# Optimization experiments

Measured on AMD Instinct MI355X. Metric: run time of the kernel, lower is better.

## Reference

```python
import jax, jax.numpy as jnp
import numpy as np

N_QUBITS = 10
BATCH = 16384
Q_DEPTH = 2


def _apply_1q_shared(state, U, q):
    # state: [B, 2, 2, ..., 2]; U: [2, 2] complex, acting on wire q
    state = jnp.moveaxis(state, 1 + q, -1)
    state = jnp.einsum('b...i,ji->b...j', state, U)
    return jnp.moveaxis(state, -1, 1 + q)


def _apply_ry_batched(state, angles, q):
    # per-sample RY(angle) on wire q; angles: [B] float
    c = jnp.cos(angles * 0.5).astype(jnp.complex64)
    s = jnp.sin(angles * 0.5).astype(jnp.complex64)
    U = jnp.stack([jnp.stack([c, -s], -1), jnp.stack([s, c], -1)], -2)  # [B,2,2]
    state = jnp.moveaxis(state, 1 + q, -1)
    state = jnp.einsum('b...i,bji->b...j', state, U)
    return jnp.moveaxis(state, -1, 1 + q)


def _rot_matrix(phi, theta, omega):
    # PennyLane Rot = RZ(omega) @ RY(theta) @ RZ(phi)
    c = jnp.cos(theta * 0.5)
    s = jnp.sin(theta * 0.5)
    m00 = jnp.exp(-0.5j * (phi + omega)) * c
    m01 = -jnp.exp(0.5j * (phi - omega)) * s
    m10 = jnp.exp(-0.5j * (phi - omega)) * s
    m11 = jnp.exp(0.5j * (phi + omega)) * c
    return jnp.stack([jnp.stack([m00, m01]), jnp.stack([m10, m11])]).astype(jnp.complex64)


def _apply_cnot(state, c, t):
    st = jnp.moveaxis(state, (1 + c, 1 + t), (1, 2))  # [B, ctrl, tgt, ...]
    st = jnp.stack([st[:, 0], st[:, 1, ::-1]], axis=1)  # flip target where ctrl=1
    return jnp.moveaxis(st, (1, 2), (1 + c, 1 + t))


def setup_inputs() -> dict:
    key = jax.random.key(0)
    k1, k2 = jax.random.split(key)
    x = jax.random.uniform(k1, (BATCH, N_QUBITS), dtype=jnp.float32) * np.pi
    q_weights = 0.01 * jax.random.normal(k2, (Q_DEPTH, N_QUBITS, 3), dtype=jnp.float32)
    return {"x": x, "q_weights": q_weights}


def reference(x, q_weights) -> jnp.ndarray:
    B, n = x.shape
    L = q_weights.shape[0]
    # |0...0> statevector, batched: [B] + [2]*n (axis q <-> wire q, wire 0 most significant)
    state = jnp.zeros((B, 2 ** n), jnp.complex64).at[:, 0].set(1.0)
    state = state.reshape((B,) + (2,) * n)
    # AngleEmbedding(rotation='Y')
    for q in range(n):
        state = _apply_ry_batched(state, x[:, q], q)
    # StronglyEntanglingLayers: Rot on each wire, then ring of CNOTs with range (l % (n-1)) + 1
    for l in range(L):
        for q in range(n):
            U = _rot_matrix(q_weights[l, q, 0], q_weights[l, q, 1], q_weights[l, q, 2])
            state = _apply_1q_shared(state, U, q)
        r = (l % (n - 1)) + 1
        for q in range(n):
            state = _apply_cnot(state, q, (q + r) % n)
    probs = jnp.abs(state.reshape(B, 2 ** n)) ** 2  # [B, 2^n]
    bits = (np.arange(2 ** n)[:, None] >> (n - 1 - np.arange(n))[None, :]) & 1
    signs = jnp.asarray(1.0 - 2.0 * bits, jnp.float32)  # [2^n, n], PauliZ eigenvalues
    return (probs @ signs).astype(jnp.float32)  # [B, n] expvals
```

## Files before the change

kernel.cpp:

```cpp
#include <hip/hip_runtime.h>

#define DEVINL __device__ __forceinline__

typedef float f32x2 __attribute__((ext_vector_type(2)));

struct GC { int laneXor, regXor, rowL, rowR; };
struct Circ { GC g[20]; int sgnL[10], sgnR[10]; int lsel[5]; };

constexpr Circ build_circ() {
    Circ c{};
    unsigned A[10] = {};
    for (int i = 0; i < 10; ++i) A[i] = 1u << i;
    for (int w = 0; w < 10; ++w) {
        int pos = 9 - w;
        unsigned m = 1u << pos;
        c.g[w] = GC{ int(m >> 5), int(m & 31u), int(m >> 5), int(m & 31u) };
    }
    for (int q = 0; q < 10; ++q) { int pc = 9 - q, pt = 9 - ((q + 1) % 10); A[pt] ^= A[pc]; }
    unsigned M[10] = {}, Inv[10] = {};
    for (int i = 0; i < 10; ++i) { M[i] = A[i]; Inv[i] = 1u << i; }
    for (int col = 0; col < 10; ++col) {
        int piv = col;
        while (!((M[piv] >> col) & 1u)) ++piv;
        unsigned tm = M[col]; M[col] = M[piv]; M[piv] = tm;
        unsigned ti = Inv[col]; Inv[col] = Inv[piv]; Inv[piv] = ti;
        for (int r = 0; r < 10; ++r)
            if (r != col && ((M[r] >> col) & 1u)) { M[r] ^= M[col]; Inv[r] ^= Inv[col]; }
    }
    for (int w = 0; w < 10; ++w) {
        int pos = 9 - w;
        unsigned m = 0;
        for (int i = 0; i < 10; ++i) m |= ((Inv[i] >> pos) & 1u) << i;
        unsigned row = A[pos];
        c.g[10 + w] = GC{ int(m >> 5), int(m & 31u), int(row >> 5), int(row & 31u) };
    }
    for (int q = 0; q < 10; ++q) { int pc = 9 - q, pt = 9 - ((q + 2) % 10); A[pt] ^= A[pc]; }
    for (int q = 0; q < 10; ++q) { unsigned row = A[9 - q]; c.sgnL[q] = int(row >> 5); c.sgnR[q] = int(row & 31u); }

    unsigned Ucols[5] = {};
    {
        unsigned tgt[5] = {16, 8, 7, 2, 1};
        unsigned acc = 0;
        for (int k = 0; k < 5; ++k) { acc ^= tgt[k]; Ucols[k] = acc; }
    }
    unsigned Urows[5] = {};
    for (int r = 0; r < 5; ++r)
        for (int cc = 0; cc < 5; ++cc)
            Urows[r] |= ((Ucols[cc] >> r) & 1u) << cc;
    unsigned MM[5] = {}, AI[5] = {};
    for (int i = 0; i < 5; ++i) { MM[i] = Urows[i]; AI[i] = 1u << i; }
    for (int col = 0; col < 5; ++col) {
        int piv = col;
        while (!((MM[piv] >> col) & 1u)) ++piv;
        unsigned tm = MM[col]; MM[col] = MM[piv]; MM[piv] = tm;
        unsigned ti = AI[col]; AI[col] = AI[piv]; AI[piv] = ti;
        for (int r = 0; r < 5; ++r)
            if (r != col && ((MM[r] >> col) & 1u)) { MM[r] ^= MM[col]; AI[r] ^= AI[col]; }
    }
    for (int w = 0; w < 10; ++w) {
        unsigned mL = unsigned(c.g[10 + w].laneXor);
        unsigned nm = 0;
        for (int i = 0; i < 5; ++i) if ((mL >> i) & 1u) nm ^= Ucols[i];
        c.g[10 + w].laneXor = int(nm);
        unsigned rL = unsigned(c.g[10 + w].rowL);
        unsigned nr = 0;
        for (int i = 0; i < 5; ++i) if ((rL >> i) & 1u) nr ^= AI[i];
        c.g[10 + w].rowL = int(nr);
    }
    for (int q = 0; q < 10; ++q) {
        unsigned sL = unsigned(c.sgnL[q]);
        unsigned ns = 0;
        for (int i = 0; i < 5; ++i) if ((sL >> i) & 1u) ns ^= AI[i];
        c.sgnL[q] = int(ns);
    }
    for (int o = 0; o < 5; ++o) c.lsel[o] = int(AI[o]);
    return c;
}

constexpr Circ CC = build_circ();

static_assert(CC.g[10].laneXor == 1  && CC.g[10].regXor == 0,  "w0");
static_assert(CC.g[11].laneXor == 2  && CC.g[11].regXor == 0,  "w1");
static_assert(CC.g[12].laneXor == 7  && CC.g[12].regXor == 0,  "w2");
static_assert(CC.g[13].laneXor == 8  && CC.g[13].regXor == 0,  "w3");
static_assert(CC.g[14].laneXor == 16 && CC.g[14].regXor == 16, "w4");
static_assert(CC.g[15].laneXor == 0  && CC.g[15].regXor == 24, "w5");
static_assert(CC.g[16].laneXor == 0  && CC.g[16].regXor == 12, "w6");
static_assert(CC.g[17].laneXor == 0  && CC.g[17].regXor == 6,  "w7");
static_assert(CC.g[18].laneXor == 0  && CC.g[18].regXor == 3,  "w8");
static_assert(CC.g[19].laneXor == 1  && CC.g[19].regXor == 1,  "w9");
static_assert(CC.g[10].rowR == 31, "w0 rowR");
static_assert(CC.g[11].rowR == 0,  "w1 rowR");
static_assert(CC.g[12].rowR == 0,  "w2 rowR");
static_assert(CC.g[13].rowR == 0,  "w3 rowR");
static_assert(CC.g[14].rowR == 0,  "w4 rowR");
static_assert(CC.g[15].rowR == 16, "w5 rowR");
static_assert(CC.g[16].rowR == 24, "w6 rowR");
static_assert(CC.g[17].rowR == 28, "w7 rowR");
static_assert(CC.g[18].rowR == 30, "w8 rowR");
static_assert(CC.g[19].rowR == 31, "w9 rowR");

DEVINL float csw(float v, int sw) {
    return __int_as_float(__float_as_int(v) ^ sw);
}

template<int XOR>
DEVINL float fetch(float v, int lane) {
    if constexpr (XOR == 0)      return v;
    else if constexpr (XOR == 1) return __int_as_float(__builtin_amdgcn_update_dpp(0, __float_as_int(v), 0xB1, 0xF, 0xF, true));
    else if constexpr (XOR == 2) return __int_as_float(__builtin_amdgcn_update_dpp(0, __float_as_int(v), 0x4E, 0xF, 0xF, true));
    else if constexpr (XOR == 3) return __int_as_float(__builtin_amdgcn_update_dpp(0, __float_as_int(v), 0x1B, 0xF, 0xF, true));
    else if constexpr (XOR == 7) return __int_as_float(__builtin_amdgcn_update_dpp(0, __float_as_int(v), 0x141, 0xF, 0xF, true));
    else if constexpr (XOR == 8) return __int_as_float(__builtin_amdgcn_update_dpp(0, __float_as_int(v), 0x128, 0xF, 0xF, true));
    else                         return __int_as_float(__builtin_amdgcn_ds_swizzle(__float_as_int(v), 0x1F | (XOR << 10)));
}

DEVINL void pk_fma_acc(f32x2& a, f32x2 t, f32x2 b) {
    asm("v_pk_fma_f32 %0, %1, %2, %0" : "+v"(a) : "v"(t), "v"(b));
}

DEVINL f32x2 cmul(f32x2 a, f32x2 b) {
    f32x2 r;
    r.x = a.x * b.x - a.y * b.y;
    r.y = a.x * b.y + a.y * b.x;
    return r;
}

__device__ __attribute__((aligned(16))) float g_cst[80];

__global__ void qprep(const float* __restrict__ qw) {
    int g = threadIdx.x;
    if (g < 10) {
        float phi = qw[g * 3 + 0], th = qw[g * 3 + 1], om = qw[g * 3 + 2];
        float c = cosf(0.5f * th), s = sinf(0.5f * th);
        float apo = 0.5f * (phi + om), amo = 0.5f * (phi - om);
        g_cst[g * 4 + 0] =  cosf(apo) * c;
        g_cst[g * 4 + 1] = -sinf(apo) * c;
        g_cst[g * 4 + 2] = -cosf(amo) * s;
        g_cst[g * 4 + 3] = -sinf(amo) * s;
    } else if (g < 20) {
        int w = g - 10;
        float phi = qw[g * 3 + 0], th = qw[g * 3 + 1];
        float c = cosf(0.5f * th), s = sinf(0.5f * th);
        g_cst[40 + w] = s / c;
        g_cst[50 + w * 2 + 0] =  cosf(0.5f * phi);
        g_cst[50 + w * 2 + 1] = -sinf(0.5f * phi);
    } else if (g == 20) {
        float p = 1.f;
        for (int w = 0; w < 10; ++w) p *= cosf(0.5f * qw[(10 + w) * 3 + 1]);
        g_cst[70] = p;
    }
}

DEVINL void wf(const float* cst, float xw, int w, f32x2& f0, f32x2& f1) {
    float h = 0.5f * xw;
    float s = __sinf(h), c = __cosf(h);
    float m0 = cst[w * 4 + 0], m1 = cst[w * 4 + 1], m2 = cst[w * 4 + 2], m3 = cst[w * 4 + 3];
    f0.x =  m0 * c + m2 * s;
    f0.y =  m1 * c + m3 * s;
    f1.x = -m2 * c + m0 * s;
    f1.y =  m3 * c - m1 * s;
}

template<int W>
DEVINL void apply_gate(f32x2 (&a2)[32], const float* cst, int lane, const int (&sw)[10]) {
    constexpr GC gc = CC.g[10 + W];
    float tt = csw(cst[40 + W], sw[W]);
    f32x2 tp; tp.x = tt;  tp.y = tt;
    f32x2 tn; tn.x = -tt; tn.y = -tt;
    if constexpr (gc.laneXor == 0) {
        #pragma unroll
        for (int r = 0; r < 32; ++r) {
            const int r2 = r ^ gc.regXor;
            if (r < r2) {
                f32x2 old = a2[r];
                const bool sR  = __builtin_popcount(unsigned(gc.rowR & r )) & 1;
                const bool sR2 = __builtin_popcount(unsigned(gc.rowR & r2)) & 1;
                pk_fma_acc(a2[r],  sR  ? tp : tn, a2[r2]);
                pk_fma_acc(a2[r2], sR2 ? tp : tn, old);
            }
        }
    } else {
        #pragma unroll
        for (int c = 0; c < 2; ++c) {
            f32x2 b2[16];
            #pragma unroll
            for (int i = 0; i < 16; ++i) {
                const int r = (i & 7) + c * 8 + ((i >> 3) << 4);
                f32x2 s = a2[r ^ gc.regXor];
                b2[i].x = fetch<gc.laneXor>(s.x, lane);
                b2[i].y = fetch<gc.laneXor>(s.y, lane);
            }
            #pragma unroll
            for (int i = 0; i < 16; ++i) {
                const int r = (i & 7) + c * 8 + ((i >> 3) << 4);
                const bool sR = __builtin_popcount(unsigned(gc.rowR & r)) & 1;
                pk_fma_acc(a2[r], sR ? tp : tn, b2[i]);
            }
        }
    }
}

__global__ __launch_bounds__(256) void qsim(const float* __restrict__ x,
                                            float* __restrict__ out, int B) {
    const float* cst = g_cst;
    int lane = threadIdx.x & 63;
    int l5 = lane & 31;
    int b = blockIdx.x * 8 + (threadIdx.x >> 5);
    if (b >= B) return;
    const float* xb = x + b * 10;

    int sw_[10];
    #pragma unroll
    for (int w = 0; w < 10; ++w)
        sw_[w] = (__popc(unsigned(l5 & CC.g[10 + w].rowL)) & 1) << 31;

    f32x2 t01[4], t23[4], f5t[2];
    {
        f32x2 a0, a1, b0, b1;
        wf(cst, xb[9], 9, a0, a1);
        wf(cst, xb[8], 8, b0, b1);
        t01[0] = cmul(a0, b0); t01[1] = cmul(a1, b0);
        t01[2] = cmul(a0, b1); t01[3] = cmul(a1, b1);
        wf(cst, xb[7], 7, a0, a1);
        wf(cst, xb[6], 6, b0, b1);
        t23[0] = cmul(a0, b0); t23[1] = cmul(a1, b0);
        t23[2] = cmul(a0, b1); t23[3] = cmul(a1, b1);
        wf(cst, xb[5], 5, f5t[0], f5t[1]);
    }

    f32x2 E0; E0.x = cst[50];      E0.y = csw(cst[51], sw_[0]);
    f32x2 E1; E1.x = cst[52];      E1.y = csw(cst[53], sw_[1]);
    f32x2 E2; E2.x = cst[54];      E2.y = csw(cst[55], sw_[2]);
    f32x2 E3; E3.x = cst[56];      E3.y = csw(cst[57], sw_[3]);
    f32x2 E4; E4.x = cst[58];      E4.y = csw(cst[59], sw_[4]);
    f32x2 E5; E5.x = cst[60];      E5.y = csw(cst[61], sw_[5]);
    f32x2 E6; E6.x = cst[62];      E6.y = csw(cst[63], sw_[6]);
    f32x2 E7; E7.x = cst[64];      E7.y = csw(cst[65], sw_[7]);
    f32x2 E8; E8.x = cst[66];      E8.y = csw(cst[67], sw_[8]);
    f32x2 E9; E9.x = cst[68];      E9.y = csw(cst[69], sw_[9]);

    f32x2 lf;
    {
        f32x2 ea = cmul(cmul(E1, E2), cmul(E3, E4));
        float sc = cst[70];
        lf.x = ea.x * sc; lf.y = ea.y * sc;
        #pragma unroll
        for (int jj = 0; jj < 5; ++jj) {
            int w = 4 - jj;
            f32x2 f0, f1;
            wf(cst, xb[w], w, f0, f1);
            int bit = __popc(unsigned(l5 & CC.lsel[jj])) & 1;
            f32x2 p; p.x = bit ? f1.x : f0.x; p.y = bit ? f1.y : f0.y;
            lf = cmul(lf, p);
        }
    }

    f32x2 f5p[2];
    f5p[0] = cmul(f5t[0], E5);
    { f32x2 e5c; e5c.x = E5.x; e5c.y = -E5.y; f5p[1] = cmul(f5t[1], e5c); }
    f32x2 V00 = cmul(E6, E7);
    f32x2 V01; { f32x2 e7c; e7c.x = E7.x; e7c.y = -E7.y; V01 = cmul(E6, e7c); }
    f32x2 EB = cmul(E9, E0);
    f32x2 H0 = cmul(E8, EB);
    f32x2 H1; { f32x2 ebc; ebc.x = EB.x; ebc.y = -EB.y; H1 = cmul(E8, ebc); }

    f32x2 tf[8];
    #pragma unroll
    for (int j = 0; j < 8; ++j) {
        f32x2 tA = cmul(t23[j & 3], f5p[j >> 2]);
        const int s6 = ((j >> 2) ^ (j >> 1)) & 1;
        const int s7 = s6 ^ (j & 1);
        f32x2 V;
        V.x = s6 ? (s7 ? V00.x : V01.x) : (s7 ? V01.x : V00.x);
        V.y = s6 ? -(s7 ? V00.y : V01.y) : (s7 ? V01.y : V00.y);
        tf[j] = cmul(tA, V);
    }

    f32x2 g4[4];
    #pragma unroll
    for (int v = 0; v < 4; ++v) g4[v] = cmul(lf, t01[v]);
    f32x2 a2[32];
    #pragma unroll
    for (int r = 0; r < 32; ++r) {
        f32x2 t = cmul(g4[r & 3], tf[(r >> 2) & 7]);
        f32x2 G;
        G.x = (r & 1) ? H1.x : H0.x;
        G.y = (r & 1) ? H1.y : H0.y;
        if (__builtin_popcount(unsigned(r & 30)) & 1) G.y = -G.y;
        a2[r] = cmul(t, G);
    }

    apply_gate<4>(a2, cst, lane, sw_);
    apply_gate<5>(a2, cst, lane, sw_);
    apply_gate<0>(a2, cst, lane, sw_);
    apply_gate<6>(a2, cst, lane, sw_);
    apply_gate<1>(a2, cst, lane, sw_);
    apply_gate<7>(a2, cst, lane, sw_);
    apply_gate<2>(a2, cst, lane, sw_);
    apply_gate<8>(a2, cst, lane, sw_);
    apply_gate<3>(a2, cst, lane, sw_);
    apply_gate<9>(a2, cst, lane, sw_);

    float wv[32];
    #pragma unroll
    for (int r = 0; r < 32; ++r) wv[r] = a2[r].x * a2[r].x + a2[r].y * a2[r].y;
    #pragma unroll
    for (int bS = 1; bS < 16; bS <<= 1) {
        #pragma unroll
        for (int r = 0; r < 32; ++r) {
            if (!(r & bS)) {
                float xv = wv[r], yv = wv[r | bS];
                wv[r]      = xv + yv;
                wv[r | bS] = xv - yv;
            }
        }
    }

    float e[10];
    #pragma unroll
    for (int q = 0; q < 10; ++q) {
        const int R = CC.sgnR[q];
        float num = (R & 16) ? (wv[R ^ 16] - wv[R]) : (wv[R] + wv[R ^ 16]);
        int slq = __popc(unsigned(l5 & CC.sgnL[q])) & 1;
        e[q] = csw(num, slq << 31);
    }

    #pragma unroll
    for (int q = 0; q < 10; ++q) {
        e[q] += fetch<1>(e[q], lane);
        e[q] += fetch<2>(e[q], lane);
    }
    int s = l5 & 3;
    bool s1 = (s & 1) != 0, s2 = (s & 2) != 0;
    float v0 = s1 ? e[1] : e[0];
    float u0 = s1 ? e[3] : e[2];
    v0 = s2 ? u0 : v0;
    float v1 = s1 ? e[5] : e[4];
    float u1 = s1 ? e[7] : e[6];
    v1 = s2 ? u1 : v1;
    float v2 = s1 ? e[9] : e[8];

    v0 += fetch<4>(v0, lane);   v1 += fetch<4>(v1, lane);   v2 += fetch<4>(v2, lane);
    v0 += fetch<8>(v0, lane);   v1 += fetch<8>(v1, lane);   v2 += fetch<8>(v2, lane);
    v0 += fetch<16>(v0, lane);  v1 += fetch<16>(v1, lane);  v2 += fetch<16>(v2, lane);

    float vo = v0;
    int hi = l5 >> 2;
    vo = (hi == 1) ? v1 : vo;
    vo = (hi == 2) ? v2 : vo;
    if (l5 < 10) out[b * 10 + l5] = vo;
}

extern "C" void kernel_launch(void* const* d_in, const int* in_sizes, int n_in,
                              void* d_out, int out_size, void* d_ws, size_t ws_size,
                              hipStream_t stream) {
    const float* x  = (const float*)d_in[0];
    const float* qw = (const float*)d_in[1];
    float* out = (float*)d_out;
    int B = in_sizes[0] / 10;
    int blocks = (B + 7) / 8;
    hipLaunchKernelGGL(qprep, dim3(1), dim3(64), 0, stream, qw);
    hipLaunchKernelGGL(qsim, dim3(blocks), dim3(256), 0, stream, x, out, B);
}
```

Measured before the change: 84.56 us.

## Spread statevector across full 64-lane wavefront and process two samples per wave

The 1024-amplitude statevector was split as 32 lanes × 32 registers. It is now split as 64 lanes × 16 registers, and each wavefront simulates two batch samples interleaved. The constexpr qubit-to-lane/register mapping is rebuilt for 6 lane bits, and gates that cross the 32-lane boundary use bpermute or permlane32 swaps. The intent is fewer registers per sample and independent work from the second sample to hide cross-lane shuffle latency. The cost is more cross-lane traffic, including slower 32-lane exchanges, and a reduction that runs over 64 lanes.

```diff
diff --git a/kernel.cpp b/kernel.cpp
--- a/kernel.cpp
+++ b/kernel.cpp
@@ -5,7 +5,7 @@
 typedef float f32x2 __attribute__((ext_vector_type(2)));
 
 struct GC { int laneXor, regXor, rowL, rowR; };
-struct Circ { GC g[20]; int sgnL[10], sgnR[10]; int lsel[5]; };
+struct Circ { GC g[20]; int sgnL[10], sgnR[10]; int lsel[6]; };
 
 constexpr Circ build_circ() {
     Circ c{};
@@ -14,7 +14,7 @@
     for (int w = 0; w < 10; ++w) {
         int pos = 9 - w;
         unsigned m = 1u << pos;
-        c.g[w] = GC{ int(m >> 5), int(m & 31u), int(m >> 5), int(m & 31u) };
+        c.g[w] = GC{ int(m >> 4), int(m & 15u), int(m >> 4), int(m & 15u) };
     }
     for (int q = 0; q < 10; ++q) { int pc = 9 - q, pt = 9 - ((q + 1) % 10); A[pt] ^= A[pc]; }
     unsigned M[10] = {}, Inv[10] = {};
@@ -32,48 +32,48 @@
         unsigned m = 0;
         for (int i = 0; i < 10; ++i) m |= ((Inv[i] >> pos) & 1u) << i;
         unsigned row = A[pos];
-        c.g[10 + w] = GC{ int(m >> 5), int(m & 31u), int(row >> 5), int(row & 31u) };
+        c.g[10 + w] = GC{ int(m >> 4), int(m & 15u), int(row >> 4), int(row & 15u) };
     }
     for (int q = 0; q < 10; ++q) { int pc = 9 - q, pt = 9 - ((q + 2) % 10); A[pt] ^= A[pc]; }
-    for (int q = 0; q < 10; ++q) { unsigned row = A[9 - q]; c.sgnL[q] = int(row >> 5); c.sgnR[q] = int(row & 31u); }
-
-    unsigned Ucols[5] = {};
+    for (int q = 0; q < 10; ++q) { unsigned row = A[9 - q]; c.sgnL[q] = int(row >> 4); c.sgnR[q] = int(row & 15u); }
+
+    unsigned Ucols[6] = {};
     {
-        unsigned tgt[5] = {16, 8, 7, 2, 1};
+        unsigned tgt[6] = {32, 16, 7, 8, 2, 1};
         unsigned acc = 0;
-        for (int k = 0; k < 5; ++k) { acc ^= tgt[k]; Ucols[k] = acc; }
-    }
-    unsigned Urows[5] = {};
-    for (int r = 0; r < 5; ++r)
-        for (int cc = 0; cc < 5; ++cc)
+        for (int k = 0; k < 6; ++k) { acc ^= tgt[k]; Ucols[k] = acc; }
+    }
+    unsigned Urows[6] = {};
+    for (int r = 0; r < 6; ++r)
+        for (int cc = 0; cc < 6; ++cc)
             Urows[r] |= ((Ucols[cc] >> r) & 1u) << cc;
-    unsigned MM[5] = {}, AI[5] = {};
-    for (int i = 0; i < 5; ++i) { MM[i] = Urows[i]; AI[i] = 1u << i; }
-    for (int col = 0; col < 5; ++col) {
+    unsigned MM[6] = {}, AI[6] = {};
+    for (int i = 0; i < 6; ++i) { MM[i] = Urows[i]; AI[i] = 1u << i; }
+    for (int col = 0; col < 6; ++col) {
         int piv = col;
         while (!((MM[piv] >> col) & 1u)) ++piv;
         unsigned tm = MM[col]; MM[col] = MM[piv]; MM[piv] = tm;
         unsigned ti = AI[col]; AI[col] = AI[piv]; AI[piv] = ti;
-        for (int r = 0; r < 5; ++r)
+        for (int r = 0; r < 6; ++r)
             if (r != col && ((MM[r] >> col) & 1u)) { MM[r] ^= MM[col]; AI[r] ^= AI[col]; }
     }
     for (int w = 0; w < 10; ++w) {
         unsigned mL = unsigned(c.g[10 + w].laneXor);
         unsigned nm = 0;
-        for (int i = 0; i < 5; ++i) if ((mL >> i) & 1u) nm ^= Ucols[i];
+        for (int i = 0; i < 6; ++i) if ((mL >> i) & 1u) nm ^= Ucols[i];
         c.g[10 + w].laneXor = int(nm);
         unsigned rL = unsigned(c.g[10 + w].rowL);
         unsigned nr = 0;
-        for (int i = 0; i < 5; ++i) if ((rL >> i) & 1u) nr ^= AI[i];
+        for (int i = 0; i < 6; ++i) if ((rL >> i) & 1u) nr ^= AI[i];
         c.g[10 + w].rowL = int(nr);
     }
     for (int q = 0; q < 10; ++q) {
         unsigned sL = unsigned(c.sgnL[q]);
         unsigned ns = 0;
-        for (int i = 0; i < 5; ++i) if ((sL >> i) & 1u) ns ^= AI[i];
+        for (int i = 0; i < 6; ++i) if ((sL >> i) & 1u) ns ^= AI[i];
         c.sgnL[q] = int(ns);
     }
-    for (int o = 0; o < 5; ++o) c.lsel[o] = int(AI[o]);
+    for (int o = 0; o < 6; ++o) c.lsel[o] = int(AI[o]);
     return c;
 }
 
@@ -81,27 +81,41 @@
 
 static_assert(CC.g[10].laneXor == 1  && CC.g[10].regXor == 0,  "w0");
 static_assert(CC.g[11].laneXor == 2  && CC.g[11].regXor == 0,  "w1");
-static_assert(CC.g[12].laneXor == 7  && CC.g[12].regXor == 0,  "w2");
-static_assert(CC.g[13].laneXor == 8  && CC.g[13].regXor == 0,  "w3");
-static_assert(CC.g[14].laneXor == 16 && CC.g[14].regXor == 16, "w4");
-static_assert(CC.g[15].laneXor == 0  && CC.g[15].regXor == 24, "w5");
+static_assert(CC.g[12].laneXor == 8  && CC.g[12].regXor == 0,  "w2");
+static_assert(CC.g[13].laneXor == 7  && CC.g[13].regXor == 0,  "w3");
+static_assert(CC.g[14].laneXor == 16 && CC.g[14].regXor == 0,  "w4");
+static_assert(CC.g[15].laneXor == 32 && CC.g[15].regXor == 8,  "w5");
 static_assert(CC.g[16].laneXor == 0  && CC.g[16].regXor == 12, "w6");
 static_assert(CC.g[17].laneXor == 0  && CC.g[17].regXor == 6,  "w7");
 static_assert(CC.g[18].laneXor == 0  && CC.g[18].regXor == 3,  "w8");
 static_assert(CC.g[19].laneXor == 1  && CC.g[19].regXor == 1,  "w9");
-static_assert(CC.g[10].rowR == 31, "w0 rowR");
+static_assert(CC.g[10].rowR == 15, "w0 rowR");
 static_assert(CC.g[11].rowR == 0,  "w1 rowR");
 static_assert(CC.g[12].rowR == 0,  "w2 rowR");
 static_assert(CC.g[13].rowR == 0,  "w3 rowR");
 static_assert(CC.g[14].rowR == 0,  "w4 rowR");
-static_assert(CC.g[15].rowR == 16, "w5 rowR");
-static_assert(CC.g[16].rowR == 24, "w6 rowR");
-static_assert(CC.g[17].rowR == 28, "w7 rowR");
-static_assert(CC.g[18].rowR == 30, "w8 rowR");
-static_assert(CC.g[19].rowR == 31, "w9 rowR");
+static_assert(CC.g[15].rowR == 0,  "w5 rowR");
+static_assert(CC.g[16].rowR == 8,  "w6 rowR");
+static_assert(CC.g[17].rowR == 12, "w7 rowR");
+static_assert(CC.g[18].rowR == 14, "w8 rowR");
+static_assert(CC.g[19].rowR == 15, "w9 rowR");
+
+#if __has_builtin(__builtin_amdgcn_permlane32_swap)
+#define HAS_PL32 1
+#else
+#define HAS_PL32 0
+#endif
+#if __has_builtin(__builtin_amdgcn_permlane16_swap)
+#define HAS_PL16 1
+#else
+#define HAS_PL16 0
+#endif
 
 DEVINL float csw(float v, int sw) {
     return __int_as_float(__float_as_int(v) ^ sw);
+}
+DEVINL int sgnw(int lane, int rowL) {
+    return (__popc(unsigned(lane & rowL)) & 1) << 31;
 }
 
 template<int XOR>
@@ -112,7 +126,25 @@
     else if constexpr (XOR == 3) return __int_as_float(__builtin_amdgcn_update_dpp(0, __float_as_int(v), 0x1B, 0xF, 0xF, true));
     else if constexpr (XOR == 7) return __int_as_float(__builtin_amdgcn_update_dpp(0, __float_as_int(v), 0x141, 0xF, 0xF, true));
     else if constexpr (XOR == 8) return __int_as_float(__builtin_amdgcn_update_dpp(0, __float_as_int(v), 0x128, 0xF, 0xF, true));
-    else                         return __int_as_float(__builtin_amdgcn_ds_swizzle(__float_as_int(v), 0x1F | (XOR << 10)));
+    else if constexpr (XOR < 32) return __int_as_float(__builtin_amdgcn_ds_swizzle(__float_as_int(v), 0x1F | (XOR << 10)));
+    else                         return __int_as_float(__builtin_amdgcn_ds_bpermute((lane ^ XOR) << 2, __float_as_int(v)));
+}
+
+DEVINL float bsum16(float v, int lane) {
+#if HAS_PL16
+    auto r = __builtin_amdgcn_permlane16_swap(__float_as_int(v), __float_as_int(v), false, false);
+    return __int_as_float(r[0]) + __int_as_float(r[1]);
+#else
+    return v + fetch<16>(v, lane);
+#endif
+}
+DEVINL float bsum32(float v, int lane) {
+#if HAS_PL32
+    auto r = __builtin_amdgcn_permlane32_swap(__float_as_int(v), __float_as_int(v), false, false);
+    return __int_as_float(r[0]) + __int_as_float(r[1]);
+#else
+    return v + fetch<32>(v, lane);
+#endif
 }
 
 DEVINL void pk_fma_acc(f32x2& a, f32x2 t, f32x2 b) {
@@ -152,6 +184,13 @@
     }
 }
 
+DEVINL f32x2 mkE(const float* cst, int w, int lane) {
+    f32x2 E;
+    E.x = cst[50 + w * 2];
+    E.y = csw(cst[50 + w * 2 + 1], sgnw(lane, CC.g[10 + w].rowL));
+    return E;
+}
+
 DEVINL void wf(const float* cst, float xw, int w, f32x2& f0, f32x2& f1) {
     float h = 0.5f * xw;
     float s = __sinf(h), c = __cosf(h);
@@ -162,60 +201,8 @@
     f1.y =  m3 * c - m1 * s;
 }
 
-template<int W>
-DEVINL void apply_gate(f32x2 (&a2)[32], const float* cst, int lane, const int (&sw)[10]) {
-    constexpr GC gc = CC.g[10 + W];
-    float tt = csw(cst[40 + W], sw[W]);
-    f32x2 tp; tp.x = tt;  tp.y = tt;
-    f32x2 tn; tn.x = -tt; tn.y = -tt;
-    if constexpr (gc.laneXor == 0) {
-        #pragma unroll
-        for (int r = 0; r < 32; ++r) {
-            const int r2 = r ^ gc.regXor;
-            if (r < r2) {
-                f32x2 old = a2[r];
-                const bool sR  = __builtin_popcount(unsigned(gc.rowR & r )) & 1;
-                const bool sR2 = __builtin_popcount(unsigned(gc.rowR & r2)) & 1;
-                pk_fma_acc(a2[r],  sR  ? tp : tn, a2[r2]);
-                pk_fma_acc(a2[r2], sR2 ? tp : tn, old);
-            }
-        }
-    } else {
-        #pragma unroll
-        for (int c = 0; c < 2; ++c) {
-            f32x2 b2[16];
-            #pragma unroll
-            for (int i = 0; i < 16; ++i) {
-                const int r = (i & 7) + c * 8 + ((i >> 3) << 4);
-                f32x2 s = a2[r ^ gc.regXor];
-                b2[i].x = fetch<gc.laneXor>(s.x, lane);
-                b2[i].y = fetch<gc.laneXor>(s.y, lane);
-            }
-            #pragma unroll
-            for (int i = 0; i < 16; ++i) {
-                const int r = (i & 7) + c * 8 + ((i >> 3) << 4);
-                const bool sR = __builtin_popcount(unsigned(gc.rowR & r)) & 1;
-                pk_fma_acc(a2[r], sR ? tp : tn, b2[i]);
-            }
-        }
-    }
-}
-
-__global__ __launch_bounds__(256) void qsim(const float* __restrict__ x,
-                                            float* __restrict__ out, int B) {
-    const float* cst = g_cst;
-    int lane = threadIdx.x & 63;
-    int l5 = lane & 31;
-    int b = blockIdx.x * 8 + (threadIdx.x >> 5);
-    if (b >= B) return;
-    const float* xb = x + b * 10;
-
-    int sw_[10];
-    #pragma unroll
-    for (int w = 0; w < 10; ++w)
-        sw_[w] = (__popc(unsigned(l5 & CC.g[10 + w].rowL)) & 1) << 31;
-
-    f32x2 t01[4], t23[4], f5t[2];
+DEVINL void build_state(const float* cst, const float* xb, int lane, f32x2 (&a2)[16]) {
+    f32x2 t01[4], t23[4];
     {
         f32x2 a0, a1, b0, b1;
         wf(cst, xb[9], 9, a0, a1);
@@ -226,89 +213,143 @@
         wf(cst, xb[6], 6, b0, b1);
         t23[0] = cmul(a0, b0); t23[1] = cmul(a1, b0);
         t23[2] = cmul(a0, b1); t23[3] = cmul(a1, b1);
-        wf(cst, xb[5], 5, f5t[0], f5t[1]);
-    }
-
-    f32x2 E0; E0.x = cst[50];      E0.y = csw(cst[51], sw_[0]);
-    f32x2 E1; E1.x = cst[52];      E1.y = csw(cst[53], sw_[1]);
-    f32x2 E2; E2.x = cst[54];      E2.y = csw(cst[55], sw_[2]);
-    f32x2 E3; E3.x = cst[56];      E3.y = csw(cst[57], sw_[3]);
-    f32x2 E4; E4.x = cst[58];      E4.y = csw(cst[59], sw_[4]);
-    f32x2 E5; E5.x = cst[60];      E5.y = csw(cst[61], sw_[5]);
-    f32x2 E6; E6.x = cst[62];      E6.y = csw(cst[63], sw_[6]);
-    f32x2 E7; E7.x = cst[64];      E7.y = csw(cst[65], sw_[7]);
-    f32x2 E8; E8.x = cst[66];      E8.y = csw(cst[67], sw_[8]);
-    f32x2 E9; E9.x = cst[68];      E9.y = csw(cst[69], sw_[9]);
-
+    }
     f32x2 lf;
     {
-        f32x2 ea = cmul(cmul(E1, E2), cmul(E3, E4));
+        f32x2 ea = mkE(cst, 1, lane);
+        ea = cmul(ea, mkE(cst, 2, lane));
+        ea = cmul(ea, mkE(cst, 3, lane));
+        ea = cmul(ea, mkE(cst, 4, lane));
+        ea = cmul(ea, mkE(cst, 5, lane));
         float sc = cst[70];
         lf.x = ea.x * sc; lf.y = ea.y * sc;
         #pragma unroll
-        for (int jj = 0; jj < 5; ++jj) {
-            int w = 4 - jj;
+        for (int jj = 0; jj < 6; ++jj) {
+            int w = 5 - jj;
             f32x2 f0, f1;
             wf(cst, xb[w], w, f0, f1);
-            int bit = __popc(unsigned(l5 & CC.lsel[jj])) & 1;
+            int bit = __popc(unsigned(lane & CC.lsel[jj])) & 1;
             f32x2 p; p.x = bit ? f1.x : f0.x; p.y = bit ? f1.y : f0.y;
             lf = cmul(lf, p);
         }
     }
-
-    f32x2 f5p[2];
-    f5p[0] = cmul(f5t[0], E5);
-    { f32x2 e5c; e5c.x = E5.x; e5c.y = -E5.y; f5p[1] = cmul(f5t[1], e5c); }
-    f32x2 V00 = cmul(E6, E7);
-    f32x2 V01; { f32x2 e7c; e7c.x = E7.x; e7c.y = -E7.y; V01 = cmul(E6, e7c); }
-    f32x2 EB = cmul(E9, E0);
-    f32x2 H0 = cmul(E8, EB);
-    f32x2 H1; { f32x2 ebc; ebc.x = EB.x; ebc.y = -EB.y; H1 = cmul(E8, ebc); }
-
-    f32x2 tf[8];
-    #pragma unroll
-    for (int j = 0; j < 8; ++j) {
-        f32x2 tA = cmul(t23[j & 3], f5p[j >> 2]);
-        const int s6 = ((j >> 2) ^ (j >> 1)) & 1;
-        const int s7 = s6 ^ (j & 1);
-        f32x2 V;
-        V.x = s6 ? (s7 ? V00.x : V01.x) : (s7 ? V01.x : V00.x);
-        V.y = s6 ? -(s7 ? V00.y : V01.y) : (s7 ? V01.y : V00.y);
-        tf[j] = cmul(tA, V);
-    }
-
-    f32x2 g4[4];
-    #pragma unroll
-    for (int v = 0; v < 4; ++v) g4[v] = cmul(lf, t01[v]);
-    f32x2 a2[32];
-    #pragma unroll
-    for (int r = 0; r < 32; ++r) {
-        f32x2 t = cmul(g4[r & 3], tf[(r >> 2) & 7]);
-        f32x2 G;
-        G.x = (r & 1) ? H1.x : H0.x;
-        G.y = (r & 1) ? H1.y : H0.y;
-        if (__builtin_popcount(unsigned(r & 30)) & 1) G.y = -G.y;
-        a2[r] = cmul(t, G);
-    }
-
-    apply_gate<4>(a2, cst, lane, sw_);
-    apply_gate<5>(a2, cst, lane, sw_);
-    apply_gate<0>(a2, cst, lane, sw_);
-    apply_gate<6>(a2, cst, lane, sw_);
-    apply_gate<1>(a2, cst, lane, sw_);
-    apply_gate<7>(a2, cst, lane, sw_);
-    apply_gate<2>(a2, cst, lane, sw_);
-    apply_gate<8>(a2, cst, lane, sw_);
-    apply_gate<3>(a2, cst, lane, sw_);
-    apply_gate<9>(a2, cst, lane, sw_);
-
-    float wv[32];
-    #pragma unroll
-    for (int r = 0; r < 32; ++r) wv[r] = a2[r].x * a2[r].x + a2[r].y * a2[r].y;
-    #pragma unroll
-    for (int bS = 1; bS < 16; bS <<= 1) {
+    f32x2 E6 = mkE(cst, 6, lane), E7 = mkE(cst, 7, lane);
+    float Pr_ = E6.x * E7.x - E6.y * E7.y, Pi_ = E6.x * E7.y + E6.y * E7.x;
+    float Qr_ = E6.x * E7.x + E6.y * E7.y, Qi_ = E6.y * E7.x - E6.x * E7.y;
+    f32x2 t23p[4];
+    t23p[0].x = t23[0].x * Pr_ - t23[0].y * Pi_;  t23p[0].y = t23[0].x * Pi_ + t23[0].y * Pr_;
+    t23p[1].x = t23[1].x * Qr_ - t23[1].y * Qi_;  t23p[1].y = t23[1].x * Qi_ + t23[1].y * Qr_;
+    t23p[2].x = t23[2].x * Pr_ + t23[2].y * Pi_;  t23p[2].y = t23[2].y * Pr_ - t23[2].x * Pi_;
+    t23p[3].x = t23[3].x * Qr_ + t23[3].y * Qi_;  t23p[3].y = t23[3].y * Qr_ - t23[3].x * Qi_;
+    f32x2 E0 = mkE(cst, 0, lane), E9 = mkE(cst, 9, lane), E8 = mkE(cst, 8, lane);
+    f32x2 EB = cmul(E0, E9);
+    f32x2 G0 = cmul(E8, EB);
+    f32x2 EBc; EBc.x = EB.x; EBc.y = -EB.y;
+    f32x2 G1 = cmul(E8, EBc);
+    f32x2 g4H[4][2];
+    #pragma unroll
+    for (int v = 0; v < 4; ++v) {
+        f32x2 g = cmul(lf, t01[v]);
+        f32x2 G = (v & 1) ? G1 : G0;
+        g4H[v][0] = cmul(g, G);
+        f32x2 Gc; Gc.x = G.x; Gc.y = -G.y;
+        g4H[v][1] = cmul(g, Gc);
+    }
+    #pragma unroll
+    for (int r = 0; r < 16; ++r) {
+        const int v = r & 3, j = r >> 2;
+        const int sel = ((v >> 1) ^ j ^ (j >> 1)) & 1;
+        a2[r] = cmul(g4H[v][sel], t23p[j]);
+    }
+}
+
+template<int W>
+DEVINL void apply_gate2(f32x2 (&aA)[16], f32x2 (&aB)[16], const float* cst, int lane) {
+    constexpr GC gc = CC.g[10 + W];
+    float tt = csw(cst[40 + W], sgnw(lane, gc.rowL));
+    f32x2 tp; tp.x = tt;  tp.y = tt;
+    f32x2 tn; tn.x = -tt; tn.y = -tt;
+    if constexpr (gc.laneXor == 0) {
         #pragma unroll
-        for (int r = 0; r < 32; ++r) {
+        for (int r = 0; r < 16; ++r) {
+            const int r2 = r ^ gc.regXor;
+            if (r < r2) {
+                const bool sR  = __builtin_popcount(unsigned(gc.rowR & r )) & 1;
+                const bool sR2 = __builtin_popcount(unsigned(gc.rowR & r2)) & 1;
+                { f32x2 ca = aA[r], cb = aA[r2];
+                  aA[r]  = ca + (sR  ? tp : tn) * cb;
+                  aA[r2] = cb + (sR2 ? tp : tn) * ca; }
+                { f32x2 ca = aB[r], cb = aB[r2];
+                  aB[r]  = ca + (sR  ? tp : tn) * cb;
+                  aB[r2] = cb + (sR2 ? tp : tn) * ca; }
+            }
+        }
+    } else if constexpr (gc.regXor == 0) {
+        #pragma unroll
+        for (int ch = 0; ch < 2; ++ch) {
+            f32x2 bA[8], bB[8];
+            #pragma unroll
+            for (int i = 0; i < 8; ++i) {
+                const int r = ch * 8 + i;
+                bA[i].x = fetch<gc.laneXor>(aA[r].x, lane);
+                bA[i].y = fetch<gc.laneXor>(aA[r].y, lane);
+                bB[i].x = fetch<gc.laneXor>(aB[r].x, lane);
+                bB[i].y = fetch<gc.laneXor>(aB[r].y, lane);
+            }
+            #pragma unroll
+            for (int i = 0; i < 8; ++i) {
+                const int r = ch * 8 + i;
+                const bool sR = __builtin_popcount(unsigned(gc.rowR & r)) & 1;
+                pk_fma_acc(aA[r], sR ? tp : tn, bA[i]);
+                pk_fma_acc(aB[r], sR ? tp : tn, bB[i]);
+            }
+        }
+    } else {
+        static_assert((gc.regXor & (gc.regXor - 1)) == 0, "regXor pow2");
+        constexpr int bp = (gc.regXor == 8) ? 3 :
+                           (gc.regXor == 4) ? 2 :
+                           (gc.regXor == 2) ? 1 : 0;
+        #pragma unroll
+        for (int ch = 0; ch < 2; ++ch) {
+            f32x2 loA[4], hiA[4], loB[4], hiB[4];
+            #pragma unroll
+            for (int i = 0; i < 4; ++i) {
+                const int p  = ch * 4 + i;
+                const int lo = ((p >> bp) << (bp + 1)) | (p & (gc.regXor - 1));
+                const int hi = lo | gc.regXor;
+                loA[i].x = fetch<gc.laneXor>(aA[hi].x, lane);
+                loA[i].y = fetch<gc.laneXor>(aA[hi].y, lane);
+                hiA[i].x = fetch<gc.laneXor>(aA[lo].x, lane);
+                hiA[i].y = fetch<gc.laneXor>(aA[lo].y, lane);
+                loB[i].x = fetch<gc.laneXor>(aB[hi].x, lane);
+                loB[i].y = fetch<gc.laneXor>(aB[hi].y, lane);
+                hiB[i].x = fetch<gc.laneXor>(aB[lo].x, lane);
+                hiB[i].y = fetch<gc.laneXor>(aB[lo].y, lane);
+            }
+            #pragma unroll
+            for (int i = 0; i < 4; ++i) {
+                const int p  = ch * 4 + i;
+                const int lo = ((p >> bp) << (bp + 1)) | (p & (gc.regXor - 1));
+                const int hi = lo | gc.regXor;
+                const bool sLo = __builtin_popcount(unsigned(gc.rowR & lo)) & 1;
+                const bool sHi = __builtin_popcount(unsigned(gc.rowR & hi)) & 1;
+                pk_fma_acc(aA[lo], sLo ? tp : tn, loA[i]);
+                pk_fma_acc(aA[hi], sHi ? tp : tn, hiA[i]);
+                pk_fma_acc(aB[lo], sLo ? tp : tn, loB[i]);
+                pk_fma_acc(aB[hi], sHi ? tp : tn, hiB[i]);
+            }
+        }
+    }
+}
+
+DEVINL void expvals(const f32x2 (&a2)[16], int lane, float (&e)[10]) {
+    float wv[16];
+    #pragma unroll
+    for (int r = 0; r < 16; ++r) wv[r] = a2[r].x * a2[r].x + a2[r].y * a2[r].y;
+    #pragma unroll
+    for (int bS = 1; bS < 8; bS <<= 1) {
+        #pragma unroll
+        for (int r = 0; r < 16; ++r) {
             if (!(r & bS)) {
                 float xv = wv[r], yv = wv[r | bS];
                 wv[r]      = xv + yv;
@@ -316,40 +357,92 @@
             }
         }
     }
-
-    float e[10];
     #pragma unroll
     for (int q = 0; q < 10; ++q) {
         const int R = CC.sgnR[q];
-        float num = (R & 16) ? (wv[R ^ 16] - wv[R]) : (wv[R] + wv[R ^ 16]);
-        int slq = __popc(unsigned(l5 & CC.sgnL[q])) & 1;
+        float num = (R & 8) ? (wv[R ^ 8] - wv[R]) : (wv[R] + wv[R ^ 8]);
+        int slq = __popc(unsigned(lane & CC.sgnL[q])) & 1;
         e[q] = csw(num, slq << 31);
     }
+}
+
+__global__ __launch_bounds__(256) void qsim(const float* __restrict__ x,
+                                            float* __restrict__ out, int B) {
+    const float* cst = g_cst;
+    int lane = threadIdx.x & 63;
+    int wid = threadIdx.x >> 6;
+    int bA = blockIdx.x * 8 + wid * 2;
+    if (bA >= B) return;
+    int bB = bA + 1;
+    int bBl = (bB < B) ? bB : bA;
+
+    const f32x2* xpA = reinterpret_cast<const f32x2*>(x + bA * 10);
+    const f32x2* xpB = reinterpret_cast<const f32x2*>(x + bBl * 10);
+    f32x2 a0 = xpA[0], a1 = xpA[1], a2v = xpA[2], a3 = xpA[3], a4 = xpA[4];
+    f32x2 b0 = xpB[0], b1 = xpB[1], b2v = xpB[2], b3 = xpB[3], b4 = xpB[4];
+    float xA[10] = { a0.x, a0.y, a1.x, a1.y, a2v.x, a2v.y, a3.x, a3.y, a4.x, a4.y };
+    float xB[10] = { b0.x, b0.y, b1.x, b1.y, b2v.x, b2v.y, b3.x, b3.y, b4.x, b4.y };
+
+    f32x2 sA[16], sB[16];
+    build_state(cst, xA, lane, sA);
+    build_state(cst, xB, lane, sB);
+
+    apply_gate2<5>(sA, sB, cst, lane);
+    apply_gate2<6>(sA, sB, cst, lane);
+    apply_gate2<4>(sA, sB, cst, lane);
+    apply_gate2<7>(sA, sB, cst, lane);
+    apply_gate2<3>(sA, sB, cst, lane);
+    apply_gate2<8>(sA, sB, cst, lane);
+    apply_gate2<2>(sA, sB, cst, lane);
+    apply_gate2<1>(sA, sB, cst, lane);
+    apply_gate2<0>(sA, sB, cst, lane);
+    apply_gate2<9>(sA, sB, cst, lane);
+
+    float eA[10], eB[10];
+    expvals(sA, lane, eA);
+    expvals(sB, lane, eB);
 
     #pragma unroll
     for (int q = 0; q < 10; ++q) {
-        e[q] += fetch<1>(e[q], lane);
-        e[q] += fetch<2>(e[q], lane);
-    }
-    int s = l5 & 3;
+        eA[q] += fetch<1>(eA[q], lane);
+        eB[q] += fetch<1>(eB[q], lane);
+        eA[q] += fetch<2>(eA[q], lane);
+        eB[q] += fetch<2>(eB[q], lane);
+    }
+    int s = lane & 3;
     bool s1 = (s & 1) != 0, s2 = (s & 2) != 0;
-    float v0 = s1 ? e[1] : e[0];
-    float u0 = s1 ? e[3] : e[2];
-    v0 = s2 ? u0 : v0;
-    float v1 = s1 ? e[5] : e[4];
-    float u1 = s1 ? e[7] : e[6];
-    v1 = s2 ? u1 : v1;
-    float v2 = s1 ? e[9] : e[8];
-
-    v0 += fetch<4>(v0, lane);   v1 += fetch<4>(v1, lane);   v2 += fetch<4>(v2, lane);
-    v0 += fetch<8>(v0, lane);   v1 += fetch<8>(v1, lane);   v2 += fetch<8>(v2, lane);
-    v0 += fetch<16>(v0, lane);  v1 += fetch<16>(v1, lane);  v2 += fetch<16>(v2, lane);
-
-    float vo = v0;
-    int hi = l5 >> 2;
-    vo = (hi == 1) ? v1 : vo;
-    vo = (hi == 2) ? v2 : vo;
-    if (l5 < 10) out[b * 10 + l5] = vo;
+    float vA0 = s1 ? eA[1] : eA[0];
+    float uA0 = s1 ? eA[3] : eA[2];
+    vA0 = s2 ? uA0 : vA0;
+    float vA1 = s1 ? eA[5] : eA[4];
+    float uA1 = s1 ? eA[7] : eA[6];
+    vA1 = s2 ? uA1 : vA1;
+    float vA2 = s1 ? eA[9] : eA[8];
+    float vB0 = s1 ? eB[1] : eB[0];
+    float uB0 = s1 ? eB[3] : eB[2];
+    vB0 = s2 ? uB0 : vB0;
+    float vB1 = s1 ? eB[5] : eB[4];
+    float uB1 = s1 ? eB[7] : eB[6];
+    vB1 = s2 ? uB1 : vB1;
+    float vB2 = s1 ? eB[9] : eB[8];
+
+    vA0 += fetch<4>(vA0, lane);  vA1 += fetch<4>(vA1, lane);  vA2 += fetch<4>(vA2, lane);
+    vB0 += fetch<4>(vB0, lane);  vB1 += fetch<4>(vB1, lane);  vB2 += fetch<4>(vB2, lane);
+    vA0 += fetch<8>(vA0, lane);  vA1 += fetch<8>(vA1, lane);  vA2 += fetch<8>(vA2, lane);
+    vB0 += fetch<8>(vB0, lane);  vB1 += fetch<8>(vB1, lane);  vB2 += fetch<8>(vB2, lane);
+    vA0 = bsum16(vA0, lane);     vA1 = bsum16(vA1, lane);     vA2 = bsum16(vA2, lane);
+    vB0 = bsum16(vB0, lane);     vB1 = bsum16(vB1, lane);     vB2 = bsum16(vB2, lane);
+    vA0 = bsum32(vA0, lane);     vA1 = bsum32(vA1, lane);     vA2 = bsum32(vA2, lane);
+    vB0 = bsum32(vB0, lane);     vB1 = bsum32(vB1, lane);     vB2 = bsum32(vB2, lane);
+
+    float voA = vA0, voB = vB0;
+    int hi = lane >> 2;
+    voA = (hi == 1) ? vA1 : voA;  voA = (hi == 2) ? vA2 : voA;
+    voB = (hi == 1) ? vB1 : voB;  voB = (hi == 2) ? vB2 : voB;
+    if (lane < 10) {
+        out[bA * 10 + lane] = voA;
+        if (bB < B) out[bB * 10 + lane] = voB;
+    }
 }
 
 extern "C" void kernel_launch(void* const* d_in, const int* in_sizes, int n_in,
```

New measurement: 86.06 us. Within noise of the previous version (+1.8%).
